# Performance work log

Hardware: AMD Instinct MI355X
Metric: run time of the kernel (lower is better)

## Reference

```python
import jax, jax.numpy as jnp
import numpy as np

NUM_HEADS = 8
DIM = 256
SCALE = (DIM // NUM_HEADS) ** -0.5  # head_dim = dim // nhead = 32


def setup_inputs() -> dict:
    key = jax.random.key(0)
    k1, k2, k3, k4, k5 = jax.random.split(key, 5)
    B, N = 1, 4096
    qk = jax.random.normal(k1, (B, N, 3 * DIM), dtype=jnp.float32)
    v_cls = jax.random.normal(k2, (B, N, 2 * DIM), dtype=jnp.float32)
    masks = jax.random.uniform(k3, (B, N, N), dtype=jnp.float32)
    # torch Linear weights stored as [in, out] for x @ W
    W_qk = jax.random.normal(k4, (3 * DIM, 6 * DIM), dtype=jnp.float32) * (3 * DIM) ** -0.5
    W_v = jax.random.normal(k5, (2 * DIM, 2 * DIM), dtype=jnp.float32) * (2 * DIM) ** -0.5
    return {"qk": qk, "v_cls": v_cls, "masks": masks, "W_qk": W_qk, "W_v": W_v}


def reference(qk, v_cls, masks, W_qk, W_v):
    B, N, C_qk = qk.shape
    C_cls = v_cls.shape[-1]
    H = NUM_HEADS
    hd_qk = C_qk // H   # 96
    hd_v = C_cls // H   # 64

    # qk projection: [B,N,6*dim] -> (2,B,H,N,hd_qk)
    proj = (qk @ W_qk).reshape(B, N, 2, H, hd_qk).transpose(2, 0, 3, 1, 4)
    q, k = proj[0], proj[1]                      # [B,H,N,hd_qk]
    v = (v_cls @ W_v).reshape(B, N, H, hd_v).transpose(0, 2, 1, 3)  # [B,H,N,hd_v]

    attn = jnp.einsum('bhnd,bhmd->bhnm', q, k) * SCALE
    attn = jax.nn.softmax(attn, axis=-1)

    # post-softmax mask-mul and renorm by mask-sum and head count
    m = masks[:, None]                           # [B,1,N,N] broadcast over heads
    attn = attn * m / (H * jnp.sum(m, axis=-1, keepdims=True))
    # attn_drop with p=0.0 is identity in eval

    x_cls = jnp.einsum('bhnm,bhmd->bhnd', attn, v)
    return x_cls.transpose(0, 2, 1, 3).reshape(B, N, C_cls)
```

## Files before the change

### kernel.cpp

```cpp
#include <hip/hip_runtime.h>

typedef __attribute__((ext_vector_type(8))) _Float16 half8;
typedef __attribute__((ext_vector_type(4))) _Float16 half4;
typedef __attribute__((ext_vector_type(2))) _Float16 half2;
typedef __attribute__((ext_vector_type(2))) __fp16 fp16x2;
typedef __attribute__((ext_vector_type(4))) float f32x4;

#define N_SEQ 4096
#define HD_QK 96
#define HD_V  64
#define NHEADS 8
#define QSCALE 0.25505545556f
#define ESHIFT 8.0f

union PKC { fp16x2 p; half2 h; };

__device__ inline half2 pk_cvt(float a, float b) {
    PKC u;
    u.p = __builtin_amdgcn_cvt_pkrtz(a, b);
    return u.h;
}

__device__ inline half8 cvt8(float4 a, float4 b) {
    half8 h;
    h[0] = (_Float16)a.x; h[1] = (_Float16)a.y; h[2] = (_Float16)a.z; h[3] = (_Float16)a.w;
    h[4] = (_Float16)b.x; h[5] = (_Float16)b.y; h[6] = (_Float16)b.z; h[7] = (_Float16)b.w;
    return h;
}

__device__ inline void cast_blk(const float* __restrict__ in, _Float16* __restrict__ out,
                                int blk, int t) {
    size_t i = ((size_t)blk * 256 + t) * 8;
    float4 a = *(const float4*)(in + i);
    float4 b = *(const float4*)(in + i + 4);
    *(half8*)(out + i) = cvt8(a, b);
}

__device__ __forceinline__ void gl16(const void* g, void* l) {
    __builtin_amdgcn_global_load_lds(
        (const __attribute__((address_space(1))) unsigned int*)g,
        (__attribute__((address_space(3))) unsigned int*)l, 16, 0, 0);
}

__global__ __launch_bounds__(256) void prep(
    const float* __restrict__ qk, const float* __restrict__ v_cls,
    const float* __restrict__ masks, const float* __restrict__ W_qk,
    const float* __restrict__ W_v,
    _Float16* __restrict__ Xh, _Float16* __restrict__ Vch,
    _Float16* __restrict__ Msw, float* __restrict__ Msum,
    _Float16* __restrict__ Wqkt, _Float16* __restrict__ Wvt)
{
    __shared__ float tile[32][33];
    const int bx = blockIdx.x, t = threadIdx.x;
    if (bx < 1536) {
        cast_blk(qk, Xh, bx, t);
    } else if (bx < 2560) {
        cast_blk(v_cls, Vch, bx - 1536, t);
    } else if (bx < 3968) {
        const bool big = bx < 3712;
        const int id = big ? bx - 2560 : bx - 3712;
        const int nx = big ? 48 : 16;
        const int C = big ? 1536 : 512, R = big ? 768 : 512;
        const float* in = big ? W_qk : W_v;
        _Float16* out = big ? Wqkt : Wvt;
        int cx = id % nx, cy = id / nx;
        int tx = t & 31, ty = t >> 5;
        int c0 = cx * 32, r0 = cy * 32;
        for (int k = 0; k < 4; k++)
            tile[ty + 8 * k][tx] = in[(size_t)(r0 + ty + 8 * k) * C + c0 + tx];
        __syncthreads();
        for (int k = 0; k < 4; k++)
            out[(size_t)(c0 + ty + 8 * k) * R + r0 + tx] = (_Float16)tile[tx][ty + 8 * k];
    } else {
        const int m = bx - 3968;
        const int q = m >> 1;
        const int k0 = (m & 1) * 2048 + t * 8;
        const float* src = masks + (size_t)q * N_SEQ + k0;
        float4 a = *(const float4*)src;
        float4 b = *(const float4*)(src + 4);
        const int q0b = q >> 6, l15 = q & 15, nt = (q >> 4) & 3;
        const int kb = k0 >> 6, wsl = (k0 >> 4) & 3, qd = (k0 >> 2) & 3;
        _Float16* dst = Msw + ((size_t)(q0b * 64 + kb) * 4 + wsl) * 1024
                            + l15 * 64 + qd * 16 + nt * 4;
        half4 h0 = {(_Float16)a.x, (_Float16)a.y, (_Float16)a.z, (_Float16)a.w};
        half4 h1 = {(_Float16)b.x, (_Float16)b.y, (_Float16)b.z, (_Float16)b.w};
        *(half4*)dst = h0;
        *(half4*)(dst + 16) = h1;
        float s = (a.x + a.y) + (a.z + a.w) + (b.x + b.y) + (b.z + b.w);
        for (int off = 1; off < 64; off <<= 1) s += __shfl_xor(s, off);
        if ((t & 63) == 0) atomicAdd(&Msum[q], s);
    }
}

__global__ __launch_bounds__(256) void proj_fused(
    const _Float16* __restrict__ Xh, const _Float16* __restrict__ Vch,
    const _Float16* __restrict__ Wqkt, const _Float16* __restrict__ Wvt,
    _Float16* __restrict__ Qh, _Float16* __restrict__ Kh,
    _Float16* __restrict__ Vtg)
{
    __shared__ _Float16 smem[2 * 128 * 72];
    _Float16 (*Xs)[72] = (_Float16 (*)[72])smem;
    _Float16 (*Ws)[72] = (_Float16 (*)[72])(smem + 128 * 72);

    const int t = threadIdx.x;
    const int lane = t & 63, wv = t >> 6;
    const int quad = lane >> 4, l15 = lane & 15;
    const bool qkmode = blockIdx.x < 12;
    const int n0 = qkmode ? blockIdx.x * 128 : (blockIdx.x - 12) * 128;
    const int row0 = blockIdx.y * 128;
    const int K = qkmode ? 768 : 512;
    const _Float16* X = qkmode ? Xh : Vch;
    const _Float16* Wt = qkmode ? Wqkt : Wvt;

    const int mB = (wv & 1) * 64, nB = (wv >> 1) * 64;
    const int sr = t >> 1, sk = (t & 1) * 32;

    const f32x4 fzero = {0.f, 0.f, 0.f, 0.f};
    f32x4 acc[4][4];
    for (int i = 0; i < 4; i++)
        for (int j = 0; j < 4; j++) acc[i][j] = fzero;

    for (int k0 = 0; k0 < K; k0 += 64) {
        __syncthreads();
        {
            const _Float16* xp = X + (size_t)(row0 + sr) * K + k0 + sk;
            *(half8*)&Xs[sr][sk]      = *(const half8*)xp;
            *(half8*)&Xs[sr][sk + 8]  = *(const half8*)(xp + 8);
            *(half8*)&Xs[sr][sk + 16] = *(const half8*)(xp + 16);
            *(half8*)&Xs[sr][sk + 24] = *(const half8*)(xp + 24);
            const _Float16* wp = Wt + (size_t)(n0 + sr) * K + k0 + sk;
            *(half8*)&Ws[sr][sk]      = *(const half8*)wp;
            *(half8*)&Ws[sr][sk + 8]  = *(const half8*)(wp + 8);
            *(half8*)&Ws[sr][sk + 16] = *(const half8*)(wp + 16);
            *(half8*)&Ws[sr][sk + 24] = *(const half8*)(wp + 24);
        }
        __syncthreads();
        for (int c = 0; c < 2; c++) {
            half8 af[4], bf[4];
            for (int i = 0; i < 4; i++)
                af[i] = *(const half8*)&Xs[mB + 16 * i + l15][c * 32 + quad * 8];
            for (int j = 0; j < 4; j++)
                bf[j] = *(const half8*)&Ws[nB + 16 * j + l15][c * 32 + quad * 8];
            for (int i = 0; i < 4; i++)
                for (int j = 0; j < 4; j++)
                    acc[i][j] = __builtin_amdgcn_mfma_f32_16x16x32_f16(af[i], bf[j], acc[i][j], 0, 0, 0);
        }
    }

    __syncthreads();
    _Float16 (*Ct)[136] = (_Float16 (*)[136])smem;
    for (int j = 0; j < 4; j++) {
        int col = n0 + nB + 16 * j + l15;
        float scl = (qkmode && col < 768) ? QSCALE : 1.0f;
        for (int i = 0; i < 4; i++)
            for (int r = 0; r < 4; r++)
                Ct[mB + 16 * i + quad * 4 + r][nB + 16 * j + l15] =
                    (_Float16)(acc[i][j][r] * scl);
    }
    __syncthreads();

    if (qkmode) {
        for (int e = 0; e < 8; e++) {
            int id = e * 256 + t;
            int row = id >> 4, cc = id & 15;
            int col = n0 + cc * 8;
            int w = col >= 768 ? 1 : 0;
            int rem = col - w * 768;
            int h = rem / 96, d = rem - h * 96;
            _Float16* dst = w ? Kh : Qh;
            *(half8*)&dst[((size_t)h * N_SEQ + row0 + row) * HD_QK + d] =
                *(const half8*)&Ct[row][cc * 8];
        }
    } else {
        for (int e = 0; e < 4; e++) {
            int id = e * 256 + t;
            int col = id >> 3, rc = id & 7;
            int c = n0 + col;
            int h = c >> 6, d = c & 63;
            half8 v0, v1;
            for (int k = 0; k < 8; k++) {
                v0[k] = Ct[rc * 16 + k][col];
                v1[k] = Ct[rc * 16 + 8 + k][col];
            }
            _Float16* dst = &Vtg[((size_t)h * HD_V + d) * N_SEQ + row0 + rc * 16];
            *(half8*)dst = v0;
            *(half8*)(dst + 8) = v1;
        }
    }
}

__global__ __launch_bounds__(256, 3) void flash_attn(
    const _Float16* __restrict__ Qh, const _Float16* __restrict__ Kh,
    const _Float16* __restrict__ Vtg, const _Float16* __restrict__ Msw,
    _Float16* __restrict__ Owsh, float* __restrict__ Lws)
{
    __shared__ __align__(16) char smem[41472];

    const int t = threadIdx.x;
    const int lane = t & 63, w = t >> 6;
    const int quad = lane >> 4, l15 = lane & 15;
    const int bx = blockIdx.x;
    const int q0b = bx & 63;
    const int hz = bx >> 6;
    const int head = hz & 7;
    const int z = hz >> 3;
    const int q0 = q0b * 64;
    const int kb0 = 21 * z, kbE = (z == 2) ? 64 : kb0 + 21;

    half8 qf[3][4];
    for (int nt = 0; nt < 4; nt++) {
        const _Float16* qp = Qh + ((size_t)head * N_SEQ + q0 + 16 * nt + l15) * HD_QK + 8 * quad;
        for (int c = 0; c < 3; c++)
            qf[c][nt] = *(const half8*)(qp + 32 * c);
    }

    const char* kgb = (const char*)Kh
        + ((size_t)(head * N_SEQ + 16 * w + l15) * HD_QK + 8 * quad) * 2;
    const char* vgb = (const char*)Vtg
        + ((size_t)(head * HD_V + lane) * N_SEQ) * 2 + 32 * w;
    const _Float16* mbase = Msw + ((size_t)(q0b * 64 + kb0) * 4 + w) * 1024
                                + (l15 * 4 + quad) * 16;

    char* stW = smem + w * 10240;

    const f32x4 fzero = {0.f, 0.f, 0.f, 0.f};
    const f32x4 minit = {-ESHIFT, -ESHIFT, -ESHIFT, -ESHIFT};
    f32x4 oacc[4][4];
    for (int nt = 0; nt < 4; nt++)
        for (int v = 0; v < 4; v++) oacc[nt][v] = fzero;
    float lsum[4] = {0.f, 0.f, 0.f, 0.f};

    half8 m01, m23;

    {
        char* kd = stW;
        const char* ks = kgb + (size_t)kb0 * 12288;
        gl16(ks, kd);
        gl16(ks + 64, kd + 1024);
        gl16(ks + 128, kd + 2048);
        char* vd = stW + 3072;
        const char* vs = vgb + (size_t)kb0 * 128;
        gl16(vs, vd);
        gl16(vs + 16, vd + 1024);
    }
    m01 = *(const half8*)mbase;
    m23 = *(const half8*)(mbase + 8);

    int cur = 0;
    for (int j = kb0; j < kbE; j++, cur ^= 1) {
        asm volatile("s_waitcnt vmcnt(2)" ::: "memory");
        __builtin_amdgcn_sched_barrier(0);

        const char* kl = stW + cur * 5120;
        half8 kf[3];
        kf[0] = *(const half8*)(kl + lane * 16);
        kf[1] = *(const half8*)(kl + 1024 + lane * 16);
        kf[2] = *(const half8*)(kl + 2048 + lane * 16);
        const char* vl = kl + 3072 + (quad >> 1) * 1024 + l15 * 16 + (quad & 1) * 8;
        half4 vf[4];
        vf[0] = *(const half4*)(vl);
        vf[1] = *(const half4*)(vl + 256);
        vf[2] = *(const half4*)(vl + 512);
        vf[3] = *(const half4*)(vl + 768);

        const int jn = (j + 1 < kbE) ? j + 1 : j;
        {
            char* kd = stW + (cur ^ 1) * 5120;
            const char* ks = kgb + (size_t)jn * 12288;
            gl16(ks, kd);
            gl16(ks + 64, kd + 1024);
            gl16(ks + 128, kd + 2048);
            char* vd = kd + 3072;
            const char* vs = vgb + (size_t)jn * 128;
            gl16(vs, vd);
            gl16(vs + 16, vd + 1024);
        }

        f32x4 sT[4];
        for (int nt = 0; nt < 4; nt++) {
            f32x4 s = __builtin_amdgcn_mfma_f32_16x16x32_f16(kf[0], qf[0][nt], minit, 0, 0, 0);
            s = __builtin_amdgcn_mfma_f32_16x16x32_f16(kf[1], qf[1][nt], s, 0, 0, 0);
            s = __builtin_amdgcn_mfma_f32_16x16x32_f16(kf[2], qf[2][nt], s, 0, 0, 0);
            sT[nt] = s;
        }

        half4 af[4];
        {
            half2 mh[8];
            for (int i = 0; i < 4; i++) {
                mh[i]     = half2{m01[2 * i], m01[2 * i + 1]};
                mh[4 + i] = half2{m23[2 * i], m23[2 * i + 1]};
            }
            for (int nt = 0; nt < 4; nt++) {
                float p0 = exp2f(sT[nt][0]);
                float p1 = exp2f(sT[nt][1]);
                float p2 = exp2f(sT[nt][2]);
                float p3 = exp2f(sT[nt][3]);
                lsum[nt] += (p0 + p1) + (p2 + p3);
                half2 lo = pk_cvt(p0, p1) * mh[2 * nt];
                half2 hi = pk_cvt(p2, p3) * mh[2 * nt + 1];
                af[nt] = half4{lo[0], lo[1], hi[0], hi[1]};
            }
        }
        {
            const _Float16* mp = mbase + (size_t)(jn - kb0) * 4096;
            m01 = *(const half8*)mp;
            m23 = *(const half8*)(mp + 8);
        }

        for (int nt = 0; nt < 4; nt++)
            for (int v = 0; v < 4; v++)
                oacc[nt][v] = __builtin_amdgcn_mfma_f32_16x16x16f16(af[nt], vf[v], oacc[nt][v], 0, 0, 0);
    }

    __syncthreads();

    float (*Ob)[64][68] = (float (*)[64][68])smem;
    float (*Lb)[64] = (float (*)[64])(smem + 34816);

    for (int nt = 0; nt < 4; nt++) {
        lsum[nt] += __shfl_xor(lsum[nt], 16);
        lsum[nt] += __shfl_xor(lsum[nt], 32);
    }

    if (w & 1) {
        for (int nt = 0; nt < 4; nt++) {
            for (int v = 0; v < 4; v++)
                for (int r = 0; r < 4; r++)
                    Ob[w >> 1][16 * nt + 4 * quad + r][16 * v + l15] = oacc[nt][v][r];
            if (quad == 0) Lb[w >> 1][16 * nt + l15] = lsum[nt];
        }
    }
    __syncthreads();
    if (!(w & 1)) {
        for (int nt = 0; nt < 4; nt++) {
            for (int v = 0; v < 4; v++)
                for (int r = 0; r < 4; r++)
                    Ob[w >> 1][16 * nt + 4 * quad + r][16 * v + l15] += oacc[nt][v][r];
            if (quad == 0) Lb[w >> 1][16 * nt + l15] += lsum[nt];
        }
    }
    __syncthreads();

    {
        int row = t >> 2, c0 = (t & 3) * 16;
        _Float16* obase = Owsh + (size_t)z * N_SEQ * 512 + (size_t)(q0 + row) * 512
                          + head * HD_V + c0;
        for (int g = 0; g < 2; g++) {
            half8 h;
            for (int j2 = 0; j2 < 8; j2++)
                h[j2] = (_Float16)(Ob[0][row][c0 + 8 * g + j2] + Ob[1][row][c0 + 8 * g + j2]);
            *(half8*)(obase + 8 * g) = h;
        }
        if (t < 64)
            Lws[((size_t)z * NHEADS + head) * N_SEQ + q0 + t] = Lb[0][t] + Lb[1][t];
    }
}

__global__ __launch_bounds__(256) void finalize(
    const _Float16* __restrict__ Owsh, const float* __restrict__ Lws,
    const float* __restrict__ Msum, float* __restrict__ out)
{
    const size_t ZSTR = (size_t)N_SEQ * 512;
    size_t o = ((size_t)blockIdx.x * 256 + threadIdx.x) * 8;
    int q = (int)(o >> 9);
    int head = (int)((o & 511) >> 6);
    half8 p0 = *(const half8*)(Owsh + o);
    half8 p1 = *(const half8*)(Owsh + ZSTR + o);
    half8 p2 = *(const half8*)(Owsh + 2 * ZSTR + o);
    float l = Lws[(size_t)head * N_SEQ + q]
            + Lws[((size_t)NHEADS + head) * N_SEQ + q]
            + Lws[((size_t)2 * NHEADS + head) * N_SEQ + q];
    float inv = 1.0f / (l * (float)NHEADS * Msum[q]);
    float4 r0, r1;
    r0.x = ((float)p0[0] + (float)p1[0] + (float)p2[0]) * inv;
    r0.y = ((float)p0[1] + (float)p1[1] + (float)p2[1]) * inv;
    r0.z = ((float)p0[2] + (float)p1[2] + (float)p2[2]) * inv;
    r0.w = ((float)p0[3] + (float)p1[3] + (float)p2[3]) * inv;
    r1.x = ((float)p0[4] + (float)p1[4] + (float)p2[4]) * inv;
    r1.y = ((float)p0[5] + (float)p1[5] + (float)p2[5]) * inv;
    r1.z = ((float)p0[6] + (float)p1[6] + (float)p2[6]) * inv;
    r1.w = ((float)p0[7] + (float)p1[7] + (float)p2[7]) * inv;
    *(float4*)(out + o) = r0;
    *(float4*)(out + o + 4) = r1;
}

extern "C" void kernel_launch(void* const* d_in, const int* in_sizes, int n_in,
                              void* d_out, int out_size, void* d_ws, size_t ws_size,
                              hipStream_t stream) {
    const float* qk    = (const float*)d_in[0];
    const float* v_cls = (const float*)d_in[1];
    const float* masks = (const float*)d_in[2];
    const float* W_qk  = (const float*)d_in[3];
    const float* W_v   = (const float*)d_in[4];
    float* out = (float*)d_out;

    char* wsp = (char*)d_ws;
    _Float16* Xh   = (_Float16*)(wsp);
    _Float16* Vch  = (_Float16*)(wsp + (size_t)6291456);
    _Float16* Wqkt = (_Float16*)(wsp + (size_t)10485760);
    _Float16* Wvt  = (_Float16*)(wsp + (size_t)12845056);
    _Float16* Owsh = (_Float16*)(wsp);
    size_t off = 13631488;
    auto allocB = [&](size_t bytes) { char* p = wsp + off; off += (bytes + 255) & ~(size_t)255; return p; };
    _Float16* Qh   = (_Float16*)allocB((size_t)NHEADS * N_SEQ * HD_QK * 2);
    _Float16* Kh   = (_Float16*)allocB((size_t)NHEADS * N_SEQ * HD_QK * 2);
    _Float16* Vtg  = (_Float16*)allocB((size_t)NHEADS * HD_V * N_SEQ * 2);
    _Float16* Msw  = (_Float16*)allocB((size_t)N_SEQ * N_SEQ * 2);
    float*    Msum = (float*)allocB((size_t)N_SEQ * 4);
    float*    Lws  = (float*)allocB((size_t)3 * NHEADS * N_SEQ * 4);
    (void)ws_size;

    dim3 blk(256);
    (void)hipMemsetAsync(Msum, 0, N_SEQ * sizeof(float), stream);
    prep<<<dim3(12160), blk, 0, stream>>>(
        qk, v_cls, masks, W_qk, W_v, Xh, Vch, Msw, Msum, Wqkt, Wvt);

    proj_fused<<<dim3(16, N_SEQ / 128), blk, 0, stream>>>(
        Xh, Vch, Wqkt, Wvt, Qh, Kh, Vtg);

    flash_attn<<<dim3(1536), blk, 0, stream>>>(
        Qh, Kh, Vtg, Msw, Owsh, Lws);

    finalize<<<dim3((N_SEQ * 512) / (256 * 8)), blk, 0, stream>>>(
        Owsh, Lws, Msum, out);
}
```

Measured before the change: 274.7 us.

## Store fp16 mask row-major and read it directly with strided loads

The prep kernel now converts the mask to a plain row-major fp16 copy, with one block per row. It computes each row sum with a block reduction, which removes the swizzled scatter layout, the atomics and the memset. The attention kernel reads its mask fragments as four half4 loads from separate rows instead of two contiguous half8 loads from the pre-swizzled layout, and the wait count rises to cover the extra loads. This makes the prep writes coalesced and cheaper, at the cost of less coalesced 8-byte mask reads in the hot attention loop.

```diff
diff --git a/kernel.cpp b/kernel.cpp
--- a/kernel.cpp
+++ b/kernel.cpp
@@ -47,7 +47,7 @@
     const float* __restrict__ masks, const float* __restrict__ W_qk,
     const float* __restrict__ W_v,
     _Float16* __restrict__ Xh, _Float16* __restrict__ Vch,
-    _Float16* __restrict__ Msw, float* __restrict__ Msum,
+    _Float16* __restrict__ Mh, float* __restrict__ Msum,
     _Float16* __restrict__ Wqkt, _Float16* __restrict__ Wvt)
 {
     __shared__ float tile[32][33];
@@ -72,23 +72,22 @@
         for (int k = 0; k < 4; k++)
             out[(size_t)(c0 + ty + 8 * k) * R + r0 + tx] = (_Float16)tile[tx][ty + 8 * k];
     } else {
-        const int m = bx - 3968;
-        const int q = m >> 1;
-        const int k0 = (m & 1) * 2048 + t * 8;
-        const float* src = masks + (size_t)q * N_SEQ + k0;
-        float4 a = *(const float4*)src;
-        float4 b = *(const float4*)(src + 4);
-        const int q0b = q >> 6, l15 = q & 15, nt = (q >> 4) & 3;
-        const int kb = k0 >> 6, wsl = (k0 >> 4) & 3, qd = (k0 >> 2) & 3;
-        _Float16* dst = Msw + ((size_t)(q0b * 64 + kb) * 4 + wsl) * 1024
-                            + l15 * 64 + qd * 16 + nt * 4;
-        half4 h0 = {(_Float16)a.x, (_Float16)a.y, (_Float16)a.z, (_Float16)a.w};
-        half4 h1 = {(_Float16)b.x, (_Float16)b.y, (_Float16)b.z, (_Float16)b.w};
-        *(half4*)dst = h0;
-        *(half4*)(dst + 16) = h1;
-        float s = (a.x + a.y) + (a.z + a.w) + (b.x + b.y) + (b.z + b.w);
+        const int q = bx - 3968;
+        const float* src = masks + (size_t)q * N_SEQ + t * 16;
+        float4 a0 = *(const float4*)(src);
+        float4 a1 = *(const float4*)(src + 4);
+        float4 a2 = *(const float4*)(src + 8);
+        float4 a3 = *(const float4*)(src + 12);
+        _Float16* dst = Mh + (size_t)q * N_SEQ + t * 16;
+        *(half8*)dst = cvt8(a0, a1);
+        *(half8*)(dst + 8) = cvt8(a2, a3);
+        float s = ((a0.x + a0.y) + (a0.z + a0.w)) + ((a1.x + a1.y) + (a1.z + a1.w))
+                + ((a2.x + a2.y) + (a2.z + a2.w)) + ((a3.x + a3.y) + (a3.z + a3.w));
         for (int off = 1; off < 64; off <<= 1) s += __shfl_xor(s, off);
-        if ((t & 63) == 0) atomicAdd(&Msum[q], s);
+        if ((t & 63) == 0) tile[0][t >> 6] = s;
+        __syncthreads();
+        if (t == 0)
+            Msum[q] = (tile[0][0] + tile[0][1]) + (tile[0][2] + tile[0][3]);
     }
 }
 
@@ -191,10 +190,10 @@
 
 __global__ __launch_bounds__(256, 3) void flash_attn(
     const _Float16* __restrict__ Qh, const _Float16* __restrict__ Kh,
-    const _Float16* __restrict__ Vtg, const _Float16* __restrict__ Msw,
+    const _Float16* __restrict__ Vtg, const _Float16* __restrict__ Mh,
     _Float16* __restrict__ Owsh, float* __restrict__ Lws)
 {
-    __shared__ __align__(16) char smem[41472];
+    __shared__ __align__(16) char smem[40960];
 
     const int t = threadIdx.x;
     const int lane = t & 63, w = t >> 6;
@@ -218,8 +217,7 @@
         + ((size_t)(head * N_SEQ + 16 * w + l15) * HD_QK + 8 * quad) * 2;
     const char* vgb = (const char*)Vtg
         + ((size_t)(head * HD_V + lane) * N_SEQ) * 2 + 32 * w;
-    const _Float16* mbase = Msw + ((size_t)(q0b * 64 + kb0) * 4 + w) * 1024
-                                + (l15 * 4 + quad) * 16;
+    const _Float16* mb = Mh + (size_t)(q0 + l15) * N_SEQ + 16 * w + 4 * quad;
 
     char* stW = smem + w * 10240;
 
@@ -230,7 +228,7 @@
         for (int v = 0; v < 4; v++) oacc[nt][v] = fzero;
     float lsum[4] = {0.f, 0.f, 0.f, 0.f};
 
-    half8 m01, m23;
+    half4 m0, m1, m2, m3;
 
     {
         char* kd = stW;
@@ -243,12 +241,17 @@
         gl16(vs, vd);
         gl16(vs + 16, vd + 1024);
     }
-    m01 = *(const half8*)mbase;
-    m23 = *(const half8*)(mbase + 8);
+    {
+        const _Float16* mp = mb + (size_t)kb0 * 64;
+        m0 = *(const half4*)(mp);
+        m1 = *(const half4*)(mp + 16 * N_SEQ);
+        m2 = *(const half4*)(mp + 32 * N_SEQ);
+        m3 = *(const half4*)(mp + 48 * N_SEQ);
+    }
 
     int cur = 0;
     for (int j = kb0; j < kbE; j++, cur ^= 1) {
-        asm volatile("s_waitcnt vmcnt(2)" ::: "memory");
+        asm volatile("s_waitcnt vmcnt(4)" ::: "memory");
         __builtin_amdgcn_sched_barrier(0);
 
         const char* kl = stW + cur * 5120;
@@ -287,10 +290,10 @@
         half4 af[4];
         {
             half2 mh[8];
-            for (int i = 0; i < 4; i++) {
-                mh[i]     = half2{m01[2 * i], m01[2 * i + 1]};
-                mh[4 + i] = half2{m23[2 * i], m23[2 * i + 1]};
-            }
+            mh[0] = half2{m0[0], m0[1]}; mh[1] = half2{m0[2], m0[3]};
+            mh[2] = half2{m1[0], m1[1]}; mh[3] = half2{m1[2], m1[3]};
+            mh[4] = half2{m2[0], m2[1]}; mh[5] = half2{m2[2], m2[3]};
+            mh[6] = half2{m3[0], m3[1]}; mh[7] = half2{m3[2], m3[3]};
             for (int nt = 0; nt < 4; nt++) {
                 float p0 = exp2f(sT[nt][0]);
                 float p1 = exp2f(sT[nt][1]);
@@ -303,9 +306,11 @@
             }
         }
         {
-            const _Float16* mp = mbase + (size_t)(jn - kb0) * 4096;
-            m01 = *(const half8*)mp;
-            m23 = *(const half8*)(mp + 8);
+            const _Float16* mp = mb + (size_t)jn * 64;
+            m0 = *(const half4*)(mp);
+            m1 = *(const half4*)(mp + 16 * N_SEQ);
+            m2 = *(const half4*)(mp + 32 * N_SEQ);
+            m3 = *(const half4*)(mp + 48 * N_SEQ);
         }
 
         for (int nt = 0; nt < 4; nt++)
@@ -406,21 +411,20 @@
     _Float16* Qh   = (_Float16*)allocB((size_t)NHEADS * N_SEQ * HD_QK * 2);
     _Float16* Kh   = (_Float16*)allocB((size_t)NHEADS * N_SEQ * HD_QK * 2);
     _Float16* Vtg  = (_Float16*)allocB((size_t)NHEADS * HD_V * N_SEQ * 2);
-    _Float16* Msw  = (_Float16*)allocB((size_t)N_SEQ * N_SEQ * 2);
+    _Float16* Mh   = (_Float16*)allocB((size_t)N_SEQ * N_SEQ * 2);
     float*    Msum = (float*)allocB((size_t)N_SEQ * 4);
     float*    Lws  = (float*)allocB((size_t)3 * NHEADS * N_SEQ * 4);
     (void)ws_size;
 
     dim3 blk(256);
-    (void)hipMemsetAsync(Msum, 0, N_SEQ * sizeof(float), stream);
-    prep<<<dim3(12160), blk, 0, stream>>>(
-        qk, v_cls, masks, W_qk, W_v, Xh, Vch, Msw, Msum, Wqkt, Wvt);
+    prep<<<dim3(8064), blk, 0, stream>>>(
+        qk, v_cls, masks, W_qk, W_v, Xh, Vch, Mh, Msum, Wqkt, Wvt);
 
     proj_fused<<<dim3(16, N_SEQ / 128), blk, 0, stream>>>(
         Xh, Vch, Wqkt, Wvt, Qh, Kh, Vtg);
 
     flash_attn<<<dim3(1536), blk, 0, stream>>>(
-        Qh, Kh, Vtg, Msw, Owsh, Lws);
+        Qh, Kh, Vtg, Mh, Owsh, Lws);
 
     finalize<<<dim3((N_SEQ * 512) / (256 * 8)), blk, 0, stream>>>(
         Owsh, Lws, Msum, out);
```

Result: no change. 271.9 us (-1.0%).
